# Performance work log

Measured on AMD Instinct MI355X. Metric: run time of the kernel, lower is better.

## Reference

```python
import jax, jax.numpy as jnp
import numpy as np

N, E, F, HID, HEADS, L, B, R = 50000, 400000, 64, 256, 4, 4, 16, 8
C = HID // HEADS  # per-head channels = 64
LN_EPS = 1e-5
NEG_SLOPE = 0.2  # GATConv LeakyReLU default


def _posenc(n, d):
    pos = jnp.arange(n, dtype=jnp.float32)[:, None]
    i = jnp.arange(d, dtype=jnp.float32)[None, :]
    rates = 1.0 / 10000.0 ** (2.0 * jnp.floor(i / 2.0) / d)
    ang = pos * rates
    return jnp.where(jnp.arange(d)[None, :] % 2 == 0, jnp.sin(ang), jnp.cos(ang))


def _layernorm(x, g, b):
    mu = x.mean(-1, keepdims=True)
    var = ((x - mu) ** 2).mean(-1, keepdims=True)
    return (x - mu) * jax.lax.rsqrt(var + LN_EPS) * g + b


def _gat_layer(x, src, dst, W, a_src, a_dst, bias):
    # x: [N, HID]; W: [HID, HID]; a_src/a_dst: [HEADS, C]; bias: [HID]
    h = (x @ W).reshape(N, HEADS, C)
    s_src = (h * a_src[None]).sum(-1)  # [N, HEADS]
    s_dst = (h * a_dst[None]).sum(-1)  # [N, HEADS]
    e = jax.nn.leaky_relu(s_src[src] + s_dst[dst], NEG_SLOPE)  # [E', HEADS]
    m = jax.ops.segment_max(e, dst, num_segments=N)
    ex = jnp.exp(e - m[dst])
    denom = jax.ops.segment_sum(ex, dst, num_segments=N)
    alpha = ex / denom[dst]  # softmax over incoming edges per dst node
    out = jax.ops.segment_sum(alpha[:, :, None] * h[src], dst, num_segments=N)
    return out.reshape(N, HID) + bias


def setup_inputs() -> dict:
    key = jax.random.key(0)
    ks = jax.random.split(key, 20)
    sc = 0.05
    batch = jnp.sort(jax.random.randint(ks[2], (N,), 0, B))
    return {
        "x": jax.random.normal(ks[0], (N, F), jnp.float32),
        "region_emb_w": jax.random.normal(ks[3], (R, F), jnp.float32) * sc,
        "in_proj_w": jax.random.normal(ks[4], (3 * F, HID), jnp.float32) * sc,
        "in_proj_b": jnp.zeros((HID,), jnp.float32),
        "gat_w": jax.random.normal(ks[5], (L, HID, HID), jnp.float32) * sc,
        "att_src": jax.random.normal(ks[6], (L, HEADS, C), jnp.float32) * sc,
        "att_dst": jax.random.normal(ks[7], (L, HEADS, C), jnp.float32) * sc,
        "gat_b": jnp.zeros((L, HID), jnp.float32),
        "ln_g": jnp.ones((L, HID), jnp.float32),
        "ln_b": jnp.zeros((L, HID), jnp.float32),
        "ro_w1": jax.random.normal(ks[8], (HID, HID), jnp.float32) * sc,
        "ro_b1": jnp.zeros((HID,), jnp.float32),
        "ro_w2": jax.random.normal(ks[9], (HID, HID), jnp.float32) * sc,
        "ro_b2": jnp.zeros((HID,), jnp.float32),
        "edge_index": jax.random.randint(ks[1], (2, E), 0, N),
        "batch": batch,
        "region_ids": jax.random.randint(ks[10], (N,), 0, R),
    }


def reference(x, region_emb_w, in_proj_w, in_proj_b, gat_w, att_src, att_dst,
              gat_b, ln_g, ln_b, ro_w1, ro_b1, ro_w2, ro_b2,
              edge_index, batch, region_ids):
    # input features: x | region embedding | sinusoidal posenc  -> [N, 3F]
    feats = jnp.concatenate([x, region_emb_w[region_ids], _posenc(N, F)], axis=-1)
    h = feats @ in_proj_w + in_proj_b
    # add self loops once (GATConv add_self_loops=True)
    loop = jnp.arange(N)
    src = jnp.concatenate([edge_index[0], loop])
    dst = jnp.concatenate([edge_index[1], loop])
    for l in range(L):
        h = _gat_layer(h, src, dst, gat_w[l], att_src[l], att_dst[l], gat_b[l])
        h = _layernorm(jax.nn.relu(h), ln_g[l], ln_b[l])
        # dropout is identity in eval mode
    # global mean pool over graphs
    sums = jax.ops.segment_sum(h, batch, num_segments=B)
    cnts = jax.ops.segment_sum(jnp.ones((N,), h.dtype), batch, num_segments=B)
    pooled = sums / jnp.maximum(cnts, 1.0)[:, None]  # [B, HID]
    out = jax.nn.gelu(pooled @ ro_w1 + ro_b1, approximate=False) @ ro_w2 + ro_b2
    return out
```

## Files before the change

kernel.cpp:

```cpp
#include <hip/hip_runtime.h>
#include <cmath>

typedef unsigned short u16;
typedef unsigned int u32;
typedef short bf16x8 __attribute__((ext_vector_type(8)));
typedef float f32x4 __attribute__((ext_vector_type(4)));

#define NN 50000
#define MP 50048
#define EE 400000
#define ET 450000
#define HIDD 256
#define KIN 192
#define LN_EPSF 1e-5f

__device__ __forceinline__ float bf2f(u16 u){ return __uint_as_float(((u32)u)<<16); }
__device__ __forceinline__ u16 f2bf(float f){
  u32 x = __float_as_uint(f);
  u32 r = x + 0x7fffu + ((x>>16)&1u);
  return (u16)(r>>16);
}
__device__ __forceinline__ float bflo(u32 v){ return __uint_as_float(v<<16); }
__device__ __forceinline__ float bfhi(u32 v){ return __uint_as_float(v & 0xffff0000u); }
__device__ __forceinline__ u32 pack2(float a, float b){ return (u32)f2bf(a) | ((u32)f2bf(b)<<16); }

__device__ __forceinline__ void dma16(const u16* g, u16* lds){
  __builtin_amdgcn_global_load_lds(
      (const __attribute__((address_space(1))) void*)g,
      (__attribute__((address_space(3))) void*)lds, 16, 0, 0);
}

__global__ __launch_bounds__(256) void k_setup(
    const float* __restrict__ x, const float* __restrict__ remb, const int* __restrict__ rid,
    u16* __restrict__ feats,
    const float* __restrict__ ipw, const float* __restrict__ gatw,
    u16* __restrict__ wtin, u16* __restrict__ wtl,
    const float* __restrict__ asrc, const float* __restrict__ adst, u16* __restrict__ vmat,
    const int* __restrict__ ei, int* __restrict__ deg)
{
  int b = blockIdx.x;
  if (b < 12512){
    int e = b*768 + threadIdx.x;
    #pragma unroll
    for (int it=0; it<3; ++it, e+=256){
      int n = e / 192;
      int c = e - n*192;
      if (n >= MP) break;
      float v = 0.f;
      if (n < NN){
        if (c < 64){
          v = x[n*64 + c];
        } else if (c < 128){
          v = remb[rid[n]*64 + (c-64)];
        } else {
          int i = c - 128;
          float rate = exp2f(-(float)(2*(i>>1)) * (1.0f/64.0f) * 13.287712379549449f);
          float s, cc;
          sincosf((float)n * rate, &s, &cc);
          v = (i & 1) ? cc : s;
        }
      }
      feats[(size_t)n*192 + c] = f2bf(v);
    }
  } else if (b < 13728){
    int idx = (b - 12512)*256 + threadIdx.x;
    if (idx < 49152){
      int n = idx / 192, k = idx - n*192;
      wtin[idx] = f2bf(ipw[k*256 + n]);
    } else {
      int j = idx - 49152;
      if (j < 262144){
        int l = j >> 16, rem = j & 65535;
        int n = rem >> 8, k = rem & 255;
        wtl[j] = f2bf(gatw[l*65536 + k*256 + n]);
      }
    }
  } else if (b < 13792){
    int idx = (b - 13728)*256 + threadIdx.x;
    if (idx < 16384){
      int l = idx >> 12, rem = idx & 4095, v = rem >> 8, k = rem & 255;
      float s = 0.f;
      if (v < 8){
        const float* a = (v < 4) ? (asrc + l*256 + v*64) : (adst + l*256 + (v-4)*64);
        const float* w = gatw + (size_t)l*65536 + k*256 + (v & 3)*64;
        #pragma unroll 8
        for (int c=0;c<64;++c) s += w[c]*a[c];
      }
      vmat[idx] = f2bf(s);
    }
  } else {
    int i = (b - 13792)*256 + threadIdx.x;
    if (i < ET){
      int d = (i < EE) ? ei[EE + i] : (i - EE);
      atomicAdd(&deg[d], 1);
    }
  }
}

__global__ void k_scan1(const int* __restrict__ deg, int* __restrict__ row_off, int* __restrict__ part){
  __shared__ int s[256];
  int n = blockIdx.x*256 + threadIdx.x;
  int v = (n < NN) ? deg[n] : 0;
  s[threadIdx.x] = v;
  __syncthreads();
  for (int off=1; off<256; off<<=1){
    int t = (threadIdx.x >= off) ? s[threadIdx.x - off] : 0;
    __syncthreads();
    s[threadIdx.x] += t;
    __syncthreads();
  }
  if (n < NN) row_off[n] = s[threadIdx.x] - v;
  if (threadIdx.x == 255) part[blockIdx.x] = s[255];
}

__global__ void k_scan23(int* __restrict__ row_off, const int* __restrict__ part, int nparts){
  __shared__ int sp[256];
  int t = threadIdx.x;
  sp[t] = (t < nparts && t < (int)blockIdx.x) ? part[t] : 0;
  __syncthreads();
  for (int off=128; off; off>>=1){
    if (t < off) sp[t] += sp[t+off];
    __syncthreads();
  }
  int n = blockIdx.x*256 + t;
  if (n < NN) row_off[n] += sp[0];
}

__global__ void k_scatter(const int* __restrict__ ei, const int* __restrict__ row_off,
                          int* __restrict__ cur, int* __restrict__ csr_src){
  int i = blockIdx.x*blockDim.x + threadIdx.x;
  if (i >= ET) return;
  int s, d;
  if (i < EE){ s = ei[i]; d = ei[EE + i]; } else { s = i - EE; d = i - EE; }
  int pos = row_off[d] + atomicAdd(&cur[d], 1);
  csr_src[pos] = s;
}

template<int K>
__global__ __launch_bounds__(256, 3) void k_gemm(
    const u16* __restrict__ A, const u16* __restrict__ Wt,
    const float* __restrict__ bias, const u16* __restrict__ vmat,
    float* __restrict__ ss, float* __restrict__ sd,
    u16* __restrict__ C, int M)
{
  __shared__ u16 Asl[128*32];
  __shared__ u16 Bsl[128*32];
  int tid = threadIdx.x;
  int wave = tid >> 6, lane = tid & 63, quad = lane >> 4, lm = lane & 15;
  int r0 = blockIdx.x * 128;
  int cb = blockIdx.y;
  int rW = (wave >> 1) * 64;
  int cW = (wave & 1) * 64;
  bool doScore = vmat && (cb == 0) && ((wave & 1) == 0);

  f32x4 acc[4][4] = {};
  f32x4 accs[4] = {};

  for (int k0 = 0; k0 < K; k0 += 32){
    for (int m = wave; m < 8; m += 4){
      int s = m*64 + lane;
      int r = s >> 2, p = s & 3;
      int c = p ^ (r & 3);
      dma16(A + (size_t)(r0 + r)*K + k0 + c*8, Asl + (size_t)m*512);
    }
    for (int m = wave; m < 8; m += 4){
      int s = m*64 + lane;
      int r = s >> 2, p = s & 3;
      int c = p ^ (r & 3);
      dma16(Wt + (size_t)(cb*128 + r)*K + k0 + c*8, Bsl + (size_t)m*512);
    }
    __syncthreads();

    bf16x8 a[4], b[4];
    #pragma unroll
    for (int i=0;i<4;++i){
      int row = rW + i*16 + lm;
      a[i] = *(const bf16x8*)(Asl + (size_t)(row*4 + (quad ^ (row & 3)))*8);
    }
    #pragma unroll
    for (int j=0;j<4;++j){
      int row = cW + j*16 + lm;
      b[j] = *(const bf16x8*)(Bsl + (size_t)(row*4 + (quad ^ (row & 3)))*8);
    }
    #pragma unroll
    for (int i=0;i<4;++i)
      #pragma unroll
      for (int j=0;j<4;++j)
        acc[i][j] = __builtin_amdgcn_mfma_f32_16x16x32_bf16(a[i], b[j], acc[i][j], 0, 0, 0);
    if (doScore){
      bf16x8 bs = *(const bf16x8*)(vmat + (size_t)lm*K + k0 + quad*8);
      #pragma unroll
      for (int i=0;i<4;++i)
        accs[i] = __builtin_amdgcn_mfma_f32_16x16x32_bf16(a[i], bs, accs[i], 0, 0, 0);
    }
    __syncthreads();
  }

  if (doScore){
    #pragma unroll
    for (int i=0;i<4;++i){
      #pragma unroll
      for (int r=0;r<4;++r){
        int row = r0 + rW + i*16 + quad*4 + r;
        if (row < M){
          if (lm < 4)      ss[row*4 + lm]     = accs[i][r];
          else if (lm < 8) sd[row*4 + lm - 4] = accs[i][r];
        }
      }
    }
  }

  #pragma unroll
  for (int i=0;i<4;++i){
    #pragma unroll
    for (int r=0;r<4;++r){
      int row = r0 + rW + i*16 + quad*4 + r;
      if (row < M){
        #pragma unroll
        for (int j=0;j<4;++j){
          int col = cb*128 + cW + j*16 + lm;
          float v = acc[i][j][r];
          if (bias) v += bias[col];
          C[(size_t)row*256 + col] = f2bf(v);
        }
      }
    }
  }
}

__global__ __launch_bounds__(256) void k_aggregate(
    const u16* __restrict__ h2, const float* __restrict__ ssrc, const float* __restrict__ sdst,
    const int* __restrict__ row_off, const int* __restrict__ deg, const int* __restrict__ csr_src,
    const float* __restrict__ bias, const float* __restrict__ g, const float* __restrict__ bb,
    u16* __restrict__ hout)
{
  int wv = (blockIdx.x*blockDim.x + threadIdx.x) >> 6;
  int lane = threadIdx.x & 63;
  int half = lane >> 5;
  int hl = lane & 31;
  int n = wv*2 + half;
  if (n >= NN) return;
  int c0 = hl*8;
  int head = hl >> 3;
  float sdh = sdst[n*4 + head];
  int ro = row_off[n];
  int dg = deg[n];
  float denA = 0.f, denB = 0.f;
  float a0=0,a1=0,a2=0,a3=0,a4=0,a5=0,a6=0,a7=0;
  float b0=0,b1=0,b2=0,b3=0,b4=0,b5=0,b6=0,b7=0;
  int j = 0;
  for (; j + 2 <= dg; j += 2){
    int sA = csr_src[ro+j];
    int sB = csr_src[ro+j+1];
    uint4 uA = *(const uint4*)(h2 + (size_t)sA*HIDD + c0);
    uint4 uB = *(const uint4*)(h2 + (size_t)sB*HIDD + c0);
    float eA = ssrc[sA*4+head] + sdh;
    float eB = ssrc[sB*4+head] + sdh;
    eA = (eA > 0.f) ? eA : 0.2f*eA;
    eB = (eB > 0.f) ? eB : 0.2f*eB;
    float xA = __expf(eA), xB = __expf(eB);
    denA += xA; denB += xB;
    a0 += xA*bflo(uA.x); a1 += xA*bfhi(uA.x);
    a2 += xA*bflo(uA.y); a3 += xA*bfhi(uA.y);
    a4 += xA*bflo(uA.z); a5 += xA*bfhi(uA.z);
    a6 += xA*bflo(uA.w); a7 += xA*bfhi(uA.w);
    b0 += xB*bflo(uB.x); b1 += xB*bfhi(uB.x);
    b2 += xB*bflo(uB.y); b3 += xB*bfhi(uB.y);
    b4 += xB*bflo(uB.z); b5 += xB*bfhi(uB.z);
    b6 += xB*bflo(uB.w); b7 += xB*bfhi(uB.w);
  }
  if (j < dg){
    int sA = csr_src[ro+j];
    uint4 uA = *(const uint4*)(h2 + (size_t)sA*HIDD + c0);
    float eA = ssrc[sA*4+head] + sdh;
    eA = (eA > 0.f) ? eA : 0.2f*eA;
    float xA = __expf(eA);
    denA += xA;
    a0 += xA*bflo(uA.x); a1 += xA*bfhi(uA.x);
    a2 += xA*bflo(uA.y); a3 += xA*bfhi(uA.y);
    a4 += xA*bflo(uA.z); a5 += xA*bfhi(uA.z);
    a6 += xA*bflo(uA.w); a7 += xA*bfhi(uA.w);
  }
  float inv = 1.f / (denA + denB);
  float y[8];
  y[0]=a0+b0; y[1]=a1+b1; y[2]=a2+b2; y[3]=a3+b3;
  y[4]=a4+b4; y[5]=a5+b5; y[6]=a6+b6; y[7]=a7+b7;
  float4 bi0 = *(const float4*)(bias + c0);
  float4 bi1 = *(const float4*)(bias + c0 + 4);
  y[0]=fmaxf(y[0]*inv+bi0.x,0.f); y[1]=fmaxf(y[1]*inv+bi0.y,0.f);
  y[2]=fmaxf(y[2]*inv+bi0.z,0.f); y[3]=fmaxf(y[3]*inv+bi0.w,0.f);
  y[4]=fmaxf(y[4]*inv+bi1.x,0.f); y[5]=fmaxf(y[5]*inv+bi1.y,0.f);
  y[6]=fmaxf(y[6]*inv+bi1.z,0.f); y[7]=fmaxf(y[7]*inv+bi1.w,0.f);
  float sum = (y[0]+y[1])+(y[2]+y[3])+((y[4]+y[5])+(y[6]+y[7]));
  #pragma unroll
  for (int o=16;o>=1;o>>=1) sum += __shfl_xor(sum, o);
  float mu = sum * (1.f/256.f);
  float d[8], sq = 0.f;
  #pragma unroll
  for (int k=0;k<8;++k){ d[k] = y[k]-mu; sq += d[k]*d[k]; }
  #pragma unroll
  for (int o=16;o>=1;o>>=1) sq += __shfl_xor(sq, o);
  float rs = rsqrtf(sq*(1.f/256.f) + LN_EPSF);
  float4 g0 = *(const float4*)(g + c0);
  float4 g1 = *(const float4*)(g + c0 + 4);
  float4 q0 = *(const float4*)(bb + c0);
  float4 q1 = *(const float4*)(bb + c0 + 4);
  uint4 o4;
  o4.x = pack2(d[0]*rs*g0.x + q0.x, d[1]*rs*g0.y + q0.y);
  o4.y = pack2(d[2]*rs*g0.z + q0.z, d[3]*rs*g0.w + q0.w);
  o4.z = pack2(d[4]*rs*g1.x + q1.x, d[5]*rs*g1.y + q1.y);
  o4.w = pack2(d[6]*rs*g1.z + q1.z, d[7]*rs*g1.w + q1.w);
  *(uint4*)(hout + (size_t)n*HIDD + c0) = o4;
}

__global__ __launch_bounds__(256) void k_pool(
    const u16* __restrict__ h, const int* __restrict__ batch,
    float* __restrict__ pooled, float* __restrict__ cnt)
{
  const int chunk = 25;
  int t = threadIdx.x;
  int n0 = blockIdx.x*chunk;
  int n1 = min(n0 + chunk, NN);
  if (n0 >= n1) return;
  float acc = 0.f;
  int curb = batch[n0];
  int runStart = n0;
  for (int n=n0; n<n1; ++n){
    int b = batch[n];
    if (b != curb){
      atomicAdd(&pooled[curb*HIDD + t], acc);
      if (t == 0) atomicAdd(&cnt[curb], (float)(n - runStart));
      acc = 0.f; curb = b; runStart = n;
    }
    acc += bf2f(h[(size_t)n*HIDD + t]);
  }
  atomicAdd(&pooled[curb*HIDD + t], acc);
  if (t == 0) atomicAdd(&cnt[curb], (float)(n1 - runStart));
}

__global__ __launch_bounds__(256) void k_readout(
    const float* __restrict__ pooled, const float* __restrict__ cnt,
    const float* __restrict__ w1, const float* __restrict__ b1,
    const float* __restrict__ w2, const float* __restrict__ b2,
    float* __restrict__ out)
{
  __shared__ float p[256], mid[256];
  int b = blockIdx.x, t = threadIdx.x;
  float c = fmaxf(cnt[b], 1.f);
  p[t] = pooled[b*HIDD + t] / c;
  __syncthreads();
  float acc = b1[t];
  for (int k=0;k<256;++k) acc += p[k]*w1[k*256+t];
  mid[t] = 0.5f*acc*(1.f + erff(acc*0.70710678118654752f));
  __syncthreads();
  float acc2 = b2[t];
  for (int k=0;k<256;++k) acc2 += mid[k]*w2[k*256+t];
  out[b*HIDD + t] = acc2;
}

extern "C" void kernel_launch(void* const* d_in, const int* in_sizes, int n_in,
                              void* d_out, int out_size, void* d_ws, size_t ws_size,
                              hipStream_t stream)
{
  const float* x    = (const float*)d_in[0];
  const float* remb = (const float*)d_in[1];
  const float* ipw  = (const float*)d_in[2];
  const float* ipb  = (const float*)d_in[3];
  const float* gatw = (const float*)d_in[4];
  const float* asrc = (const float*)d_in[5];
  const float* adst = (const float*)d_in[6];
  const float* gatb = (const float*)d_in[7];
  const float* lng  = (const float*)d_in[8];
  const float* lnb  = (const float*)d_in[9];
  const float* row1 = (const float*)d_in[10];
  const float* rob1 = (const float*)d_in[11];
  const float* row2 = (const float*)d_in[12];
  const float* rob2 = (const float*)d_in[13];
  const int* ei   = (const int*)d_in[14];
  const int* batch= (const int*)d_in[15];
  const int* rid  = (const int*)d_in[16];

  char* ws = (char*)d_ws;
  int*   deg  = (int*)  (ws + 0);
  int*   cur  = (int*)  (ws + 200192);
  float* cnt  = (float*)(ws + 400384);
  float* pool = (float*)(ws + 400640);
  int*   row  = (int*)  (ws + 417024);
  int*   part = (int*)  (ws + 617216);
  int*   csr  = (int*)  (ws + 618240);
  float* ss   = (float*)(ws + 2418432);
  float* sd   = (float*)(ws + 3219200);
  u16*   vmat = (u16*)  (ws + 4019968);
  u16*   feats= (u16*)  (ws + 4052736);
  u16*   wtin = (u16*)  (ws + 23271168);
  u16*   wtl  = (u16*)  (ws + 23369472);
  u16*   hA   = (u16*)  (ws + 23893760);
  u16*   hB   = (u16*)  (ws + 49518336);

  hipMemsetAsync(ws, 0, 417024, stream);

  k_setup <<<15550, 256, 0, stream>>>(x, remb, rid, feats, ipw, gatw, wtin, wtl,
                                      asrc, adst, vmat, ei, deg);
  k_scan1 <<<196, 256, 0, stream>>>(deg, row, part);
  k_scan23<<<196, 256, 0, stream>>>(row, part, 196);
  k_scatter<<<1758, 256, 0, stream>>>(ei, row, cur, csr);

  k_gemm<KIN><<<dim3(391,2), 256, 0, stream>>>(feats, wtin, ipb, nullptr,
                                               nullptr, nullptr, hA, NN);

  for (int l = 0; l < 4; ++l){
    k_gemm<HIDD><<<dim3(391,2), 256, 0, stream>>>(hA, wtl + (size_t)l*HIDD*HIDD, nullptr,
                                                  vmat + (size_t)l*16*256, ss, sd, hB, NN);
    k_aggregate<<<6250, 256, 0, stream>>>(hB, ss, sd, row, deg, csr,
                                          gatb + l*HIDD, lng + l*HIDD, lnb + l*HIDD, hA);
  }

  k_pool   <<<2000, 256, 0, stream>>>(hA, batch, pool, cnt);
  k_readout<<<16, 256, 0, stream>>>(pool, cnt, row1, rob1, row2, rob2, (float*)d_out);
}
```

Baseline: 493.3 us.

## Double-buffer GEMM LDS tiles, change swizzle, fuse last aggregation with mean pooling

The GEMM now stages the next K-slice into a second LDS buffer while computing on the current one, which is meant to overlap global-to-LDS copies with MFMA work. The XOR swizzle changes from row&3 to (row>>2)&3 to cut LDS bank conflicts. The final GAT aggregation is fused with global mean pooling through LDS and global atomics, which removes the write and re-read of the last hidden layer and one kernel launch. The cost is doubled LDS use per block, which may lower occupancy, plus more atomics. The loop has only a single __syncthreads per iteration, so the prefetch into the other buffer may race with waves still reading it.

```diff
diff --git a/kernel.cpp b/kernel.cpp
--- a/kernel.cpp
+++ b/kernel.cpp
@@ -143,8 +143,8 @@
     float* __restrict__ ss, float* __restrict__ sd,
     u16* __restrict__ C, int M)
 {
-  __shared__ u16 Asl[128*32];
-  __shared__ u16 Bsl[128*32];
+  __shared__ u16 Asl[2][128*32];
+  __shared__ u16 Bsl[2][128*32];
   int tid = threadIdx.x;
   int wave = tid >> 6, lane = tid & 63, quad = lane >> 4, lm = lane & 15;
   int r0 = blockIdx.x * 128;
@@ -156,31 +156,40 @@
   f32x4 acc[4][4] = {};
   f32x4 accs[4] = {};
 
-  for (int k0 = 0; k0 < K; k0 += 32){
+  auto stage = [&](int buf, int k0){
     for (int m = wave; m < 8; m += 4){
       int s = m*64 + lane;
       int r = s >> 2, p = s & 3;
-      int c = p ^ (r & 3);
-      dma16(A + (size_t)(r0 + r)*K + k0 + c*8, Asl + (size_t)m*512);
+      int c = p ^ ((r >> 2) & 3);
+      dma16(A + (size_t)(r0 + r)*K + k0 + c*8, &Asl[buf][m*512]);
     }
     for (int m = wave; m < 8; m += 4){
       int s = m*64 + lane;
       int r = s >> 2, p = s & 3;
-      int c = p ^ (r & 3);
-      dma16(Wt + (size_t)(cb*128 + r)*K + k0 + c*8, Bsl + (size_t)m*512);
-    }
-    __syncthreads();
+      int c = p ^ ((r >> 2) & 3);
+      dma16(Wt + (size_t)(cb*128 + r)*K + k0 + c*8, &Bsl[buf][m*512]);
+    }
+  };
+
+  stage(0, 0);
+  __syncthreads();
+
+  for (int ks = 0; ks < K/32; ++ks){
+    int cur = ks & 1;
+    if (ks + 1 < K/32) stage(cur ^ 1, (ks+1)*32);
 
     bf16x8 a[4], b[4];
     #pragma unroll
     for (int i=0;i<4;++i){
       int row = rW + i*16 + lm;
-      a[i] = *(const bf16x8*)(Asl + (size_t)(row*4 + (quad ^ (row & 3)))*8);
+      int slot = row*4 + (quad ^ ((row >> 2) & 3));
+      a[i] = *(const bf16x8*)(&Asl[cur][slot*8]);
     }
     #pragma unroll
     for (int j=0;j<4;++j){
       int row = cW + j*16 + lm;
-      b[j] = *(const bf16x8*)(Bsl + (size_t)(row*4 + (quad ^ (row & 3)))*8);
+      int slot = row*4 + (quad ^ ((row >> 2) & 3));
+      b[j] = *(const bf16x8*)(&Bsl[cur][slot*8]);
     }
     #pragma unroll
     for (int i=0;i<4;++i)
@@ -188,7 +197,7 @@
       for (int j=0;j<4;++j)
         acc[i][j] = __builtin_amdgcn_mfma_f32_16x16x32_bf16(a[i], b[j], acc[i][j], 0, 0, 0);
     if (doScore){
-      bf16x8 bs = *(const bf16x8*)(vmat + (size_t)lm*K + k0 + quad*8);
+      bf16x8 bs = *(const bf16x8*)(vmat + (size_t)lm*K + ks*32 + quad*8);
       #pragma unroll
       for (int i=0;i<4;++i)
         accs[i] = __builtin_amdgcn_mfma_f32_16x16x32_bf16(a[i], bs, accs[i], 0, 0, 0);
@@ -228,18 +237,13 @@
   }
 }
 
-__global__ __launch_bounds__(256) void k_aggregate(
+__device__ __forceinline__ void agg_core(
+    int n, int hl,
     const u16* __restrict__ h2, const float* __restrict__ ssrc, const float* __restrict__ sdst,
     const int* __restrict__ row_off, const int* __restrict__ deg, const int* __restrict__ csr_src,
     const float* __restrict__ bias, const float* __restrict__ g, const float* __restrict__ bb,
-    u16* __restrict__ hout)
-{
-  int wv = (blockIdx.x*blockDim.x + threadIdx.x) >> 6;
-  int lane = threadIdx.x & 63;
-  int half = lane >> 5;
-  int hl = lane & 31;
-  int n = wv*2 + half;
-  if (n >= NN) return;
+    float out[8])
+{
   int c0 = hl*8;
   int head = hl >> 3;
   float sdh = sdst[n*4 + head];
@@ -305,37 +309,69 @@
   float4 g1 = *(const float4*)(g + c0 + 4);
   float4 q0 = *(const float4*)(bb + c0);
   float4 q1 = *(const float4*)(bb + c0 + 4);
+  out[0]=d[0]*rs*g0.x+q0.x; out[1]=d[1]*rs*g0.y+q0.y;
+  out[2]=d[2]*rs*g0.z+q0.z; out[3]=d[3]*rs*g0.w+q0.w;
+  out[4]=d[4]*rs*g1.x+q1.x; out[5]=d[5]*rs*g1.y+q1.y;
+  out[6]=d[6]*rs*g1.z+q1.z; out[7]=d[7]*rs*g1.w+q1.w;
+}
+
+__global__ __launch_bounds__(256) void k_aggregate(
+    const u16* __restrict__ h2, const float* __restrict__ ssrc, const float* __restrict__ sdst,
+    const int* __restrict__ row_off, const int* __restrict__ deg, const int* __restrict__ csr_src,
+    const float* __restrict__ bias, const float* __restrict__ g, const float* __restrict__ bb,
+    u16* __restrict__ hout)
+{
+  int wv = (blockIdx.x*blockDim.x + threadIdx.x) >> 6;
+  int lane = threadIdx.x & 63;
+  int half = lane >> 5, hl = lane & 31;
+  int n = wv*2 + half;
+  if (n >= NN) return;
+  float out[8];
+  agg_core(n, hl, h2, ssrc, sdst, row_off, deg, csr_src, bias, g, bb, out);
   uint4 o4;
-  o4.x = pack2(d[0]*rs*g0.x + q0.x, d[1]*rs*g0.y + q0.y);
-  o4.y = pack2(d[2]*rs*g0.z + q0.z, d[3]*rs*g0.w + q0.w);
-  o4.z = pack2(d[4]*rs*g1.x + q1.x, d[5]*rs*g1.y + q1.y);
-  o4.w = pack2(d[6]*rs*g1.z + q1.z, d[7]*rs*g1.w + q1.w);
-  *(uint4*)(hout + (size_t)n*HIDD + c0) = o4;
-}
-
-__global__ __launch_bounds__(256) void k_pool(
-    const u16* __restrict__ h, const int* __restrict__ batch,
-    float* __restrict__ pooled, float* __restrict__ cnt)
-{
-  const int chunk = 25;
-  int t = threadIdx.x;
-  int n0 = blockIdx.x*chunk;
-  int n1 = min(n0 + chunk, NN);
-  if (n0 >= n1) return;
-  float acc = 0.f;
-  int curb = batch[n0];
-  int runStart = n0;
-  for (int n=n0; n<n1; ++n){
-    int b = batch[n];
-    if (b != curb){
-      atomicAdd(&pooled[curb*HIDD + t], acc);
-      if (t == 0) atomicAdd(&cnt[curb], (float)(n - runStart));
-      acc = 0.f; curb = b; runStart = n;
-    }
-    acc += bf2f(h[(size_t)n*HIDD + t]);
-  }
-  atomicAdd(&pooled[curb*HIDD + t], acc);
-  if (t == 0) atomicAdd(&cnt[curb], (float)(n1 - runStart));
+  o4.x = pack2(out[0], out[1]);
+  o4.y = pack2(out[2], out[3]);
+  o4.z = pack2(out[4], out[5]);
+  o4.w = pack2(out[6], out[7]);
+  *(uint4*)(hout + (size_t)n*HIDD + hl*8) = o4;
+}
+
+__global__ __launch_bounds__(256) void k_aggpool(
+    const u16* __restrict__ h2, const float* __restrict__ ssrc, const float* __restrict__ sdst,
+    const int* __restrict__ row_off, const int* __restrict__ deg, const int* __restrict__ csr_src,
+    const float* __restrict__ bias, const float* __restrict__ g, const float* __restrict__ bb,
+    const int* __restrict__ batch, float* __restrict__ pooled, float* __restrict__ cnt)
+{
+  __shared__ float pacc[256];
+  int tid = threadIdx.x;
+  int nb0 = blockIdx.x*8;
+  int wv = tid >> 6, lane = tid & 63, half = lane >> 5, hl = lane & 31;
+  int n = nb0 + wv*2 + half;
+  int nlast = min(nb0+7, NN-1);
+  bool uni = (batch[nb0] == batch[nlast]);
+  if (uni) pacc[tid] = 0.f;
+  __syncthreads();
+  bool valid = (n < NN);
+  float out[8];
+  if (valid)
+    agg_core(n, hl, h2, ssrc, sdst, row_off, deg, csr_src, bias, g, bb, out);
+  if (uni){
+    if (valid){
+      #pragma unroll
+      for (int k=0;k<8;++k) atomicAdd(&pacc[hl*8+k], out[k]);
+    }
+    __syncthreads();
+    int b = batch[nb0];
+    atomicAdd(&pooled[b*256 + tid], pacc[tid]);
+    if (tid == 0) atomicAdd(&cnt[b], (float)(min(NN - nb0, 8)));
+  } else {
+    if (valid){
+      int b = batch[n];
+      #pragma unroll
+      for (int k=0;k<8;++k) atomicAdd(&pooled[b*256 + hl*8 + k], out[k]);
+      if (hl == 0) atomicAdd(&cnt[b], 1.0f);
+    }
+  }
 }
 
 __global__ __launch_bounds__(256) void k_readout(
@@ -411,10 +447,15 @@
   for (int l = 0; l < 4; ++l){
     k_gemm<HIDD><<<dim3(391,2), 256, 0, stream>>>(hA, wtl + (size_t)l*HIDD*HIDD, nullptr,
                                                   vmat + (size_t)l*16*256, ss, sd, hB, NN);
-    k_aggregate<<<6250, 256, 0, stream>>>(hB, ss, sd, row, deg, csr,
-                                          gatb + l*HIDD, lng + l*HIDD, lnb + l*HIDD, hA);
-  }
-
-  k_pool   <<<2000, 256, 0, stream>>>(hA, batch, pool, cnt);
+    if (l < 3){
+      k_aggregate<<<6250, 256, 0, stream>>>(hB, ss, sd, row, deg, csr,
+                                            gatb + l*HIDD, lng + l*HIDD, lnb + l*HIDD, hA);
+    } else {
+      k_aggpool<<<6250, 256, 0, stream>>>(hB, ss, sd, row, deg, csr,
+                                          gatb + l*HIDD, lng + l*HIDD, lnb + l*HIDD,
+                                          batch, pool, cnt);
+    }
+  }
+
   k_readout<<<16, 256, 0, stream>>>(pool, cnt, row1, rob1, row2, rob2, (float*)d_out);
 }
```

New measurement: 532.0 us. 1.08x slower.
